# Kernel optimization log

Measured on AMD Instinct MI355X. Metric: run time of the kernel, lower is better.

Reference implementation:

```python
import jax, jax.numpy as jnp
import numpy as np

B, S, DM = 2, 2048, 2048
H, DH = 16, 128
EPS = 1e-6


def rmsnorm(t, w):
    # normalize over last dim (head_dim), fp32 math
    var = jnp.mean(jnp.square(t), axis=-1, keepdims=True)
    return t * jax.lax.rsqrt(var + EPS) * w


def apply_rope(t, freqs):
    # t: (B,S,H,D); freqs: (S,1,D/2,2,2)
    b, s, h, d = t.shape
    t2 = t.reshape(b, s, h, 2, d // 2)
    t2 = jnp.moveaxis(t2, -2, -1)[..., None, :]  # (B,S,H,D/2,1,2)
    out = freqs[..., 0] * t2[..., 0] + freqs[..., 1] * t2[..., 1]  # (B,S,H,D/2,2)
    out = jnp.moveaxis(out, -1, -2).reshape(b, s, h, d)
    return out.astype(t.dtype)


def setup_inputs() -> dict:
    key = jax.random.key(0)
    ks = jax.random.split(key, 6)
    sc = 0.02
    return {
        "x": jax.random.normal(ks[0], (B, S, DM), jnp.float32),
        "rope_emb": jax.random.normal(ks[1], (S, 1, DH // 2, 2, 2), jnp.float32),
        "wq": jax.random.normal(ks[2], (DM, DM), jnp.float32) * sc,
        "wk": jax.random.normal(ks[3], (DM, DM), jnp.float32) * sc,
        "wv": jax.random.normal(ks[4], (DM, DM), jnp.float32) * sc,
        "wo": jax.random.normal(ks[5], (DM, DM), jnp.float32) * sc,
        "q_norm_w": jnp.ones((DH,), jnp.float32),
        "k_norm_w": jnp.ones((DH,), jnp.float32),
    }


def reference(x, rope_emb, wq, wk, wv, wo, q_norm_w, k_norm_w):
    b, s, _ = x.shape
    q = (x @ wq.T).reshape(b, s, H, DH)
    k = (x @ wk.T).reshape(b, s, H, DH)
    v = (x @ wv.T).reshape(b, s, H, DH)
    q = rmsnorm(q, q_norm_w)
    k = rmsnorm(k, k_norm_w)
    q = apply_rope(q, rope_emb)
    k = apply_rope(k, rope_emb)
    scale = 1.0 / np.sqrt(DH).astype(np.float32)
    scores = jnp.einsum('bqhd,bkhd->bhqk', q, k) * scale
    attn = jax.nn.softmax(scores, axis=-1)
    out = jnp.einsum('bhqk,bkhd->bqhd', attn, v).reshape(b, s, H * DH)
    return out @ wo.T
```

## Files before the change

kernel.cpp:

```cpp
#include <hip/hip_runtime.h>

typedef __bf16 bf16x8 __attribute__((ext_vector_type(8)));
typedef __bf16 bf16x4 __attribute__((ext_vector_type(4)));
typedef float floatx4 __attribute__((ext_vector_type(4)));

#define GK 2048
#define S_LEN 2048
#define NH 16
#define DH 128

__device__ __forceinline__ void gl2lds16(const __bf16* g, __bf16* l) {
    __builtin_amdgcn_global_load_lds(
        (const __attribute__((address_space(1))) void*)g,
        (__attribute__((address_space(3))) void*)l, 16, 0, 0);
}

__global__ __launch_bounds__(256) void cvt_bf16(const float* __restrict__ in,
                                                __bf16* __restrict__ out, int n4) {
    int i = blockIdx.x * 256 + threadIdx.x;
    if (i < n4) {
        const float4 v = ((const float4*)in)[i];
        bf16x4 h;
        h[0] = (__bf16)v.x; h[1] = (__bf16)v.y; h[2] = (__bf16)v.z; h[3] = (__bf16)v.w;
        ((bf16x4*)out)[i] = h;
    }
}

__global__ __launch_bounds__(256) void cvt3_bf16(const float* __restrict__ a,
                                                 const float* __restrict__ b,
                                                 const float* __restrict__ c,
                                                 __bf16* __restrict__ out) {
    const int per = 2048 * 2048 / 4;
    int i = blockIdx.x * 256 + threadIdx.x;
    const float* src = a; int j = i;
    if (i >= 2 * per)      { src = c; j = i - 2 * per; }
    else if (i >= per)     { src = b; j = i - per; }
    const float4 v = ((const float4*)src)[j];
    bf16x4 h;
    h[0] = (__bf16)v.x; h[1] = (__bf16)v.y; h[2] = (__bf16)v.z; h[3] = (__bf16)v.w;
    ((bf16x4*)out)[i] = h;
}

__device__ __forceinline__ void gemm_body(const __bf16* __restrict__ A,
                                          const __bf16* __restrict__ W,
                                          int m0, int n0,
                                          __bf16 (*As)[32], __bf16 (*Bs)[32],
                                          floatx4 (*acc)[4]) {
    const int t = threadIdx.x, lane = t & 63, wave = t >> 6;
    const int fr = lane & 15, fq = lane >> 4;
    const int wr = (wave >> 1) * 64, wc = (wave & 1) * 64;

    const __bf16* Ap = A + (size_t)(m0 + wave * 32 + (lane >> 2)) * GK + (lane & 3) * 8;
    const __bf16* Wp = W + (size_t)(n0 + wave * 32 + (lane >> 2)) * GK + (lane & 3) * 8;
    __bf16* lA0 = &As[wave * 32][0];
    __bf16* lA1 = &As[wave * 32 + 16][0];
    __bf16* lB0 = &Bs[wave * 32][0];
    __bf16* lB1 = &Bs[wave * 32 + 16][0];

    for (int k0 = 0; k0 < GK; k0 += 32) {
        gl2lds16(Ap, lA0);
        gl2lds16(Ap + (size_t)16 * GK, lA1);
        gl2lds16(Wp, lB0);
        gl2lds16(Wp + (size_t)16 * GK, lB1);
        Ap += 32; Wp += 32;
        __syncthreads();

        bf16x8 af[4], bfg[4];
        for (int i = 0; i < 4; i++) af[i]  = *(const bf16x8*)&As[wr + i * 16 + fr][fq * 8];
        for (int j = 0; j < 4; j++) bfg[j] = *(const bf16x8*)&Bs[wc + j * 16 + fr][fq * 8];
        __builtin_amdgcn_s_setprio(1);
        for (int i = 0; i < 4; i++)
            for (int j = 0; j < 4; j++)
                acc[i][j] = __builtin_amdgcn_mfma_f32_16x16x32_bf16(af[i], bfg[j], acc[i][j], 0, 0, 0);
        __builtin_amdgcn_s_setprio(0);
        __syncthreads();
    }
}

__device__ __forceinline__ int xcd_remap(int L, int nwg) {
    return (L & 7) * (nwg >> 3) + (L >> 3);
}

__global__ __launch_bounds__(256) void gemm_qkv(const __bf16* __restrict__ A,
                                                const __bf16* __restrict__ W,
                                                __bf16* __restrict__ qb,
                                                __bf16* __restrict__ kb,
                                                __bf16* __restrict__ vbT) {
    __shared__ __align__(16) __bf16 As[128][32];
    __shared__ __align__(16) __bf16 Bs[128][32];
    const int L = blockIdx.x + (int)gridDim.x * blockIdx.y;
    const int tid2 = xcd_remap(L, (int)(gridDim.x * gridDim.y));
    const int m0 = (tid2 / (int)gridDim.x) * 128, n0 = (tid2 % (int)gridDim.x) * 128;
    floatx4 acc[4][4] = {};
    gemm_body(A, W, m0, n0, As, Bs, acc);

    const int lane = threadIdx.x & 63, wave = threadIdx.x >> 6;
    const int fr = lane & 15, fq = lane >> 4;
    const int wr = (wave >> 1) * 64, wc = (wave & 1) * 64;
    const int which = n0 >> 11;
    const int nc0 = n0 & 2047;

    for (int i = 0; i < 4; i++)
        for (int j = 0; j < 4; j++) {
            const int row = m0 + wr + i * 16 + fq * 4;
            const int col = nc0 + wc + j * 16 + fr;
            if (which == 2) {
                __bf16* Cp = vbT + (((size_t)(row & ~2047)) << 11) +
                             (size_t)col * 2048 + (row & 2047);
                bf16x4 hv;
                for (int r = 0; r < 4; r++) hv[r] = (__bf16)acc[i][j][r];
                *(bf16x4*)Cp = hv;
            } else {
                __bf16* dst = which ? kb : qb;
                for (int r = 0; r < 4; r++)
                    dst[(size_t)(row + r) * 2048 + col] = (__bf16)acc[i][j][r];
            }
        }
}

__global__ __launch_bounds__(256) void gemm_out(const __bf16* __restrict__ A,
                                                const __bf16* __restrict__ W,
                                                float* __restrict__ C) {
    __shared__ __align__(16) __bf16 As[128][32];
    __shared__ __align__(16) __bf16 Bs[128][32];
    const int L = blockIdx.x + (int)gridDim.x * blockIdx.y;
    const int tid2 = xcd_remap(L, (int)(gridDim.x * gridDim.y));
    const int m0 = (tid2 / (int)gridDim.x) * 128, n0 = (tid2 % (int)gridDim.x) * 128;
    floatx4 acc[4][4] = {};
    gemm_body(A, W, m0, n0, As, Bs, acc);

    const int lane = threadIdx.x & 63, wave = threadIdx.x >> 6;
    const int fr = lane & 15, fq = lane >> 4;
    const int wr = (wave >> 1) * 64, wc = (wave & 1) * 64;
    for (int i = 0; i < 4; i++)
        for (int j = 0; j < 4; j++) {
            const int row = m0 + wr + i * 16 + fq * 4;
            const int col = n0 + wc + j * 16 + fr;
            for (int r = 0; r < 4; r++)
                C[(size_t)(row + r) * 2048 + col] = acc[i][j][r];
        }
}

__global__ __launch_bounds__(256) void rmsrope(__bf16* __restrict__ qb,
                                               __bf16* __restrict__ kb,
                                               const float* __restrict__ rope,
                                               const float* __restrict__ qw,
                                               const float* __restrict__ kw) {
    const int lane = threadIdx.x & 63;
    const int row = blockIdx.x * 4 + (threadIdx.x >> 6);
    __bf16* p = (blockIdx.y ? kb : qb) + (size_t)row * DH;
    const float* w = blockIdx.y ? kw : qw;
    const int s = (row >> 4) & (S_LEN - 1);

    float t0 = (float)p[lane];
    float t1 = (float)p[lane + 64];
    float ss = t0 * t0 + t1 * t1;
    for (int o = 32; o; o >>= 1) ss += __shfl_xor(ss, o, 64);
    const float inv = rsqrtf(ss * (1.0f / 128.0f) + 1e-6f);
    t0 *= inv * w[lane];
    t1 *= inv * w[lane + 64];

    const float4 f = *(const float4*)(rope + (size_t)s * 256 + lane * 4);
    p[lane]      = (__bf16)(f.x * t0 + f.y * t1);
    p[lane + 64] = (__bf16)(f.z * t0 + f.w * t1);
}

__global__ __launch_bounds__(256) void flash(const __bf16* __restrict__ Q,
                                             const __bf16* __restrict__ K,
                                             const __bf16* __restrict__ Vt_g,
                                             __bf16* __restrict__ O) {
    __shared__ __align__(16) __bf16 Ks[32][136];
    __shared__ __align__(16) __bf16 Vt[144][40];
    __shared__ __align__(16) __bf16 Ps[4][32][40];

    const int t = threadIdx.x, lane = t & 63, wave = t >> 6;
    const int fr = lane & 15, fq = lane >> 4;

    const int n = blockIdx.x + (int)gridDim.x * blockIdx.y;
    const int by = (n & 7) * 4 + (n >> 7);
    const int bx = (n >> 3) & 15;
    const int b = by >> 4, h = by & 15;

    const size_t baseQ = (size_t)b * S_LEN * 2048 + h * 128;
    const size_t baseV = (size_t)b * 2048 * 2048 + (size_t)h * 128 * 2048;
    const int q0 = bx * 128 + wave * 32;
    const float sc2 = 0.08838834764831845f * 1.4426950408889634f;
    const float M2 = 12.0f * 1.4426950408889634f;

    for (int idx = t; idx < 16 * 40; idx += 256) {
        const int rr = idx / 40, cc = idx - rr * 40;
        Vt[128 + rr][cc] = (rr == 0) ? (__bf16)1.0f : (__bf16)0.0f;
    }

    bf16x8 qf[2][4];
    for (int i2 = 0; i2 < 2; i2++) {
        const __bf16* qp = Q + baseQ + (size_t)(q0 + i2 * 16 + fr) * 2048 + fq * 8;
        for (int c = 0; c < 4; c++) qf[i2][c] = *(const bf16x8*)(qp + c * 32);
    }

    floatx4 oa[2][9] = {};

    const __bf16* Kp = K + baseQ + (size_t)(t >> 3) * 2048 + (t & 7) * 16;
    const __bf16* Vp = Vt_g + baseV + (size_t)(t >> 1) * 2048 + (t & 1) * 16;

    for (int kv0 = 0; kv0 < S_LEN; kv0 += 32) {
        *(uint4*)&Ks[t >> 3][(t & 7) * 16]     = *(const uint4*)(Kp);
        *(uint4*)&Ks[t >> 3][(t & 7) * 16 + 8] = *(const uint4*)(Kp + 8);
        *(uint4*)&Vt[t >> 1][(t & 1) * 16]     = *(const uint4*)(Vp);
        *(uint4*)&Vt[t >> 1][(t & 1) * 16 + 8] = *(const uint4*)(Vp + 8);
        Kp += (size_t)32 * 2048;
        Vp += 32;
        __syncthreads();

        floatx4 sacc[2][2] = {};
        __builtin_amdgcn_s_setprio(1);
        for (int c = 0; c < 4; c++) {
            const bf16x8 kf0 = *(const bf16x8*)&Ks[fr][c * 32 + fq * 8];
            const bf16x8 kf1 = *(const bf16x8*)&Ks[fr + 16][c * 32 + fq * 8];
            sacc[0][0] = __builtin_amdgcn_mfma_f32_16x16x32_bf16(qf[0][c], kf0, sacc[0][0], 0, 0, 0);
            sacc[0][1] = __builtin_amdgcn_mfma_f32_16x16x32_bf16(qf[0][c], kf1, sacc[0][1], 0, 0, 0);
            sacc[1][0] = __builtin_amdgcn_mfma_f32_16x16x32_bf16(qf[1][c], kf0, sacc[1][0], 0, 0, 0);
            sacc[1][1] = __builtin_amdgcn_mfma_f32_16x16x32_bf16(qf[1][c], kf1, sacc[1][1], 0, 0, 0);
        }
        __builtin_amdgcn_s_setprio(0);

        for (int i2 = 0; i2 < 2; i2++)
            for (int r = 0; r < 4; r++) {
                const int row = i2 * 16 + fq * 4 + r;
                Ps[wave][row][fr]      = (__bf16)exp2f(fmaf(sc2, sacc[i2][0][r], -M2));
                Ps[wave][row][fr + 16] = (__bf16)exp2f(fmaf(sc2, sacc[i2][1][r], -M2));
            }

        const bf16x8 pf0 = *(const bf16x8*)&Ps[wave][fr][fq * 8];
        const bf16x8 pf1 = *(const bf16x8*)&Ps[wave][16 + fr][fq * 8];
        __builtin_amdgcn_s_setprio(1);
        for (int nb = 0; nb < 9; nb++) {
            const bf16x8 vf = *(const bf16x8*)&Vt[nb * 16 + fr][fq * 8];
            oa[0][nb] = __builtin_amdgcn_mfma_f32_16x16x32_bf16(pf0, vf, oa[0][nb], 0, 0, 0);
            oa[1][nb] = __builtin_amdgcn_mfma_f32_16x16x32_bf16(pf1, vf, oa[1][nb], 0, 0, 0);
        }
        __builtin_amdgcn_s_setprio(0);
        __syncthreads();
    }

    for (int i2 = 0; i2 < 2; i2++)
        for (int r = 0; r < 4; r++) {
            float l = oa[i2][8][r];
            l = __shfl(l, fq * 16);
            const float inv = 1.0f / l;
            __bf16* op = O + baseQ + (size_t)(q0 + i2 * 16 + fq * 4 + r) * 2048;
            for (int nb = 0; nb < 8; nb++)
                op[nb * 16 + fr] = (__bf16)(oa[i2][nb][r] * inv);
        }
}

extern "C" void kernel_launch(void* const* d_in, const int* in_sizes, int n_in,
                              void* d_out, int out_size, void* d_ws, size_t ws_size,
                              hipStream_t stream) {
    const float* x    = (const float*)d_in[0];
    const float* rope = (const float*)d_in[1];
    const float* wq   = (const float*)d_in[2];
    const float* wk   = (const float*)d_in[3];
    const float* wv   = (const float*)d_in[4];
    const float* wo   = (const float*)d_in[5];
    const float* qnw  = (const float*)d_in[6];
    const float* knw  = (const float*)d_in[7];
    float* out = (float*)d_out;

    const size_t NTOK = 2 * 2048;
    const size_t ELEMS = NTOK * 2048;
    __bf16* xb  = (__bf16*)d_ws;
    __bf16* qb  = xb + ELEMS;
    __bf16* kb  = qb + ELEMS;
    __bf16* vbT = kb + ELEMS;
    __bf16* ob  = xb;
    __bf16* wqkv = (__bf16*)d_out;
    __bf16* wob  = qb;

    cvt_bf16<<<(int)(ELEMS / 4) / 256, 256, 0, stream>>>(x, xb, (int)(ELEMS / 4));
    cvt3_bf16<<<3 * (2048 * 2048 / 4) / 256, 256, 0, stream>>>(wq, wk, wv, wqkv);
    gemm_qkv<<<dim3(6144 / 128, (unsigned)(NTOK / 128)), 256, 0, stream>>>(xb, wqkv, qb, kb, vbT);
    rmsrope<<<dim3((unsigned)(NTOK * 16 / 4), 2), 256, 0, stream>>>(qb, kb, rope, qnw, knw);
    flash<<<dim3(S_LEN / 128, 2 * 16), 256, 0, stream>>>(qb, kb, vbT, ob);
    cvt_bf16<<<(int)(2048 * 2048 / 4) / 256, 256, 0, stream>>>(wo, wob, 2048 * 2048 / 4);
    gemm_out<<<dim3(2048 / 128, (unsigned)(NTOK / 128)), 256, 0, stream>>>(ob, wob, out);
}
```

Measured before the change: 450.9 us.

## Rewrite GEMM mainloop with 128x256 tiles, XOR-swizzled LDS and double-buffered async loads

Replaces the single-buffered 128x128 GEMM body, which waits at a barrier on every K=32 step, with a 512-thread 128x256 tile over K=64 steps. Global-to-LDS loads are double-buffered in 96 KB of dynamic shared memory, with vmcnt waits so the next tile streams in during the MFMAs. An XOR swizzle on LDS columns is meant to avoid bank conflicts. The cost is heavy LDS use, which limits occupancy, and fewer workgroups per GEMM, which may leave compute units underused on the output projection.

```diff
diff --git a/kernel.cpp b/kernel.cpp
--- a/kernel.cpp
+++ b/kernel.cpp
@@ -10,6 +10,11 @@
 #define DH 128
 
 __device__ __forceinline__ void gl2lds16(const __bf16* g, __bf16* l) {
+    __builtin_amdgcn_global_load_lds(
+        (const __attribute__((address_space(1))) void*)g,
+        (__attribute__((address_space(3))) void*)l, 16, 0, 0);
+}
+__device__ __forceinline__ void gl2lds16c(const __bf16* g, char* l) {
     __builtin_amdgcn_global_load_lds(
         (const __attribute__((address_space(1))) void*)g,
         (__attribute__((address_space(3))) void*)l, 16, 0, 0);
@@ -41,69 +46,104 @@
     ((bf16x4*)out)[i] = h;
 }
 
-__device__ __forceinline__ void gemm_body(const __bf16* __restrict__ A,
-                                          const __bf16* __restrict__ W,
-                                          int m0, int n0,
-                                          __bf16 (*As)[32], __bf16 (*Bs)[32],
-                                          floatx4 (*acc)[4]) {
+__device__ __forceinline__ int xcd_remap(int L, int nwg) {
+    return (L & 7) * (nwg >> 3) + (L >> 3);
+}
+
+__device__ __forceinline__ void gemm_body2(const __bf16* __restrict__ A,
+                                           const __bf16* __restrict__ W,
+                                           int m0, int n0, char* lds,
+                                           floatx4 (*acc)[4]) {
     const int t = threadIdx.x, lane = t & 63, wave = t >> 6;
     const int fr = lane & 15, fq = lane >> 4;
-    const int wr = (wave >> 1) * 64, wc = (wave & 1) * 64;
-
-    const __bf16* Ap = A + (size_t)(m0 + wave * 32 + (lane >> 2)) * GK + (lane & 3) * 8;
-    const __bf16* Wp = W + (size_t)(n0 + wave * 32 + (lane >> 2)) * GK + (lane & 3) * 8;
-    __bf16* lA0 = &As[wave * 32][0];
-    __bf16* lA1 = &As[wave * 32 + 16][0];
-    __bf16* lB0 = &Bs[wave * 32][0];
-    __bf16* lB1 = &Bs[wave * 32 + 16][0];
-
-    for (int k0 = 0; k0 < GK; k0 += 32) {
-        gl2lds16(Ap, lA0);
-        gl2lds16(Ap + (size_t)16 * GK, lA1);
-        gl2lds16(Wp, lB0);
-        gl2lds16(Wp + (size_t)16 * GK, lB1);
-        Ap += 32; Wp += 32;
+    const int wm = wave >> 2, wn = wave & 3;
+    const int NKT = GK / 64;
+
+    const int swcol = ((lane & 7) * 8) ^ ((lane >> 3) * 8);
+    const __bf16* gA = A + (size_t)(m0 + wave * 8 + (lane >> 3)) * GK + swcol;
+    const __bf16* gW = W + (size_t)(n0 + wave * 8 + (lane >> 3)) * GK + swcol;
+    char* const sAw = lds + wave * 1024;
+    char* const sBw = lds + 16384 + wave * 1024;
+
+    auto STAGE = [&](int b, int kt) {
+        const __bf16* a = gA + (size_t)kt * 64;
+        const __bf16* w = gW + (size_t)kt * 64;
+        char* la = sAw + b * 49152;
+        char* lb = sBw + b * 49152;
+        gl2lds16c(a,                      la);
+        gl2lds16c(a + (size_t)64 * GK,    la + 8192);
+        gl2lds16c(w,                      lb);
+        gl2lds16c(w + (size_t)64 * GK,    lb + 8192);
+        gl2lds16c(w + (size_t)128 * GK,   lb + 16384);
+        gl2lds16c(w + (size_t)192 * GK,   lb + 24576);
+    };
+
+    STAGE(0, 0);
+    STAGE(1, 1);
+    asm volatile("s_waitcnt vmcnt(6)" ::: "memory");
+    __syncthreads();
+
+    const int sw = (fr & 7) << 4;
+    const int c0b = (fq * 16) ^ sw;
+    const int c1b = (64 + fq * 16) ^ sw;
+
+    for (int t0 = 0; t0 < NKT; t0++) {
+        const char* bufb = lds + (t0 & 1) * 49152;
+
+        bf16x8 bfr[4][2];
+#pragma unroll
+        for (int j = 0; j < 4; j++) {
+            const char* rb = bufb + 16384 + (wn * 64 + j * 16 + fr) * 128;
+            bfr[j][0] = *(const bf16x8*)(rb + c0b);
+            bfr[j][1] = *(const bf16x8*)(rb + c1b);
+        }
+#pragma unroll
+        for (int i = 0; i < 4; i++) {
+            const char* ra = bufb + (wm * 64 + i * 16 + fr) * 128;
+            const bf16x8 a0 = *(const bf16x8*)(ra + c0b);
+            const bf16x8 a1 = *(const bf16x8*)(ra + c1b);
+            __builtin_amdgcn_s_setprio(1);
+#pragma unroll
+            for (int j = 0; j < 4; j++) {
+                acc[i][j] = __builtin_amdgcn_mfma_f32_16x16x32_bf16(a0, bfr[j][0], acc[i][j], 0, 0, 0);
+                acc[i][j] = __builtin_amdgcn_mfma_f32_16x16x32_bf16(a1, bfr[j][1], acc[i][j], 0, 0, 0);
+            }
+            __builtin_amdgcn_s_setprio(0);
+        }
         __syncthreads();
-
-        bf16x8 af[4], bfg[4];
-        for (int i = 0; i < 4; i++) af[i]  = *(const bf16x8*)&As[wr + i * 16 + fr][fq * 8];
-        for (int j = 0; j < 4; j++) bfg[j] = *(const bf16x8*)&Bs[wc + j * 16 + fr][fq * 8];
-        __builtin_amdgcn_s_setprio(1);
-        for (int i = 0; i < 4; i++)
-            for (int j = 0; j < 4; j++)
-                acc[i][j] = __builtin_amdgcn_mfma_f32_16x16x32_bf16(af[i], bfg[j], acc[i][j], 0, 0, 0);
-        __builtin_amdgcn_s_setprio(0);
+        if (t0 + 2 < NKT) {
+            STAGE(t0 & 1, t0 + 2);
+            asm volatile("s_waitcnt vmcnt(6)" ::: "memory");
+        } else {
+            asm volatile("s_waitcnt vmcnt(0)" ::: "memory");
+        }
         __syncthreads();
     }
 }
 
-__device__ __forceinline__ int xcd_remap(int L, int nwg) {
-    return (L & 7) * (nwg >> 3) + (L >> 3);
-}
-
-__global__ __launch_bounds__(256) void gemm_qkv(const __bf16* __restrict__ A,
-                                                const __bf16* __restrict__ W,
-                                                __bf16* __restrict__ qb,
-                                                __bf16* __restrict__ kb,
-                                                __bf16* __restrict__ vbT) {
-    __shared__ __align__(16) __bf16 As[128][32];
-    __shared__ __align__(16) __bf16 Bs[128][32];
-    const int L = blockIdx.x + (int)gridDim.x * blockIdx.y;
-    const int tid2 = xcd_remap(L, (int)(gridDim.x * gridDim.y));
-    const int m0 = (tid2 / (int)gridDim.x) * 128, n0 = (tid2 % (int)gridDim.x) * 128;
+__global__ __launch_bounds__(512, 2) void gemm_qkv(const __bf16* __restrict__ A,
+                                                   const __bf16* __restrict__ W,
+                                                   __bf16* __restrict__ qb,
+                                                   __bf16* __restrict__ kb,
+                                                   __bf16* __restrict__ vbT) {
+    extern __shared__ __align__(16) char lds[];
+    const int gx = gridDim.x;
+    const int L = blockIdx.x + gx * blockIdx.y;
+    const int tid2 = xcd_remap(L, gx * (int)gridDim.y);
+    const int m0 = (tid2 / gx) * 128, n0 = (tid2 % gx) * 256;
     floatx4 acc[4][4] = {};
-    gemm_body(A, W, m0, n0, As, Bs, acc);
+    gemm_body2(A, W, m0, n0, lds, acc);
 
     const int lane = threadIdx.x & 63, wave = threadIdx.x >> 6;
     const int fr = lane & 15, fq = lane >> 4;
-    const int wr = (wave >> 1) * 64, wc = (wave & 1) * 64;
+    const int wm = wave >> 2, wn = wave & 3;
     const int which = n0 >> 11;
     const int nc0 = n0 & 2047;
 
     for (int i = 0; i < 4; i++)
         for (int j = 0; j < 4; j++) {
-            const int row = m0 + wr + i * 16 + fq * 4;
-            const int col = nc0 + wc + j * 16 + fr;
+            const int row = m0 + wm * 64 + i * 16 + fq * 4;
+            const int col = nc0 + wn * 64 + j * 16 + fr;
             if (which == 2) {
                 __bf16* Cp = vbT + (((size_t)(row & ~2047)) << 11) +
                              (size_t)col * 2048 + (row & 2047);
@@ -118,24 +158,24 @@
         }
 }
 
-__global__ __launch_bounds__(256) void gemm_out(const __bf16* __restrict__ A,
-                                                const __bf16* __restrict__ W,
-                                                float* __restrict__ C) {
-    __shared__ __align__(16) __bf16 As[128][32];
-    __shared__ __align__(16) __bf16 Bs[128][32];
-    const int L = blockIdx.x + (int)gridDim.x * blockIdx.y;
-    const int tid2 = xcd_remap(L, (int)(gridDim.x * gridDim.y));
-    const int m0 = (tid2 / (int)gridDim.x) * 128, n0 = (tid2 % (int)gridDim.x) * 128;
+__global__ __launch_bounds__(512, 2) void gemm_out(const __bf16* __restrict__ A,
+                                                   const __bf16* __restrict__ W,
+                                                   float* __restrict__ C) {
+    extern __shared__ __align__(16) char lds[];
+    const int gx = gridDim.x;
+    const int L = blockIdx.x + gx * blockIdx.y;
+    const int tid2 = xcd_remap(L, gx * (int)gridDim.y);
+    const int m0 = (tid2 / gx) * 128, n0 = (tid2 % gx) * 256;
     floatx4 acc[4][4] = {};
-    gemm_body(A, W, m0, n0, As, Bs, acc);
+    gemm_body2(A, W, m0, n0, lds, acc);
 
     const int lane = threadIdx.x & 63, wave = threadIdx.x >> 6;
     const int fr = lane & 15, fq = lane >> 4;
-    const int wr = (wave >> 1) * 64, wc = (wave & 1) * 64;
+    const int wm = wave >> 2, wn = wave & 3;
     for (int i = 0; i < 4; i++)
         for (int j = 0; j < 4; j++) {
-            const int row = m0 + wr + i * 16 + fq * 4;
-            const int col = n0 + wc + j * 16 + fr;
+            const int row = m0 + wm * 64 + i * 16 + fq * 4;
+            const int col = n0 + wn * 64 + j * 16 + fr;
             for (int r = 0; r < 4; r++)
                 C[(size_t)(row + r) * 2048 + col] = acc[i][j][r];
         }
@@ -279,9 +319,9 @@
 
     cvt_bf16<<<(int)(ELEMS / 4) / 256, 256, 0, stream>>>(x, xb, (int)(ELEMS / 4));
     cvt3_bf16<<<3 * (2048 * 2048 / 4) / 256, 256, 0, stream>>>(wq, wk, wv, wqkv);
-    gemm_qkv<<<dim3(6144 / 128, (unsigned)(NTOK / 128)), 256, 0, stream>>>(xb, wqkv, qb, kb, vbT);
+    gemm_qkv<<<dim3(6144 / 256, (unsigned)(NTOK / 128)), 512, 98304, stream>>>(xb, wqkv, qb, kb, vbT);
     rmsrope<<<dim3((unsigned)(NTOK * 16 / 4), 2), 256, 0, stream>>>(qb, kb, rope, qnw, knw);
     flash<<<dim3(S_LEN / 128, 2 * 16), 256, 0, stream>>>(qb, kb, vbT, ob);
     cvt_bf16<<<(int)(2048 * 2048 / 4) / 256, 256, 0, stream>>>(wo, wob, 2048 * 2048 / 4);
-    gemm_out<<<dim3(2048 / 128, (unsigned)(NTOK / 128)), 256, 0, stream>>>(ob, wob, out);
-}
+    gemm_out<<<dim3(2048 / 256, (unsigned)(NTOK / 128)), 512, 98304, stream>>>(ob, wob, out);
+}
```

Result: slower. 482.8 us (+7.1%).
